# Performance work log

Hardware: AMD Instinct MI355X
Metric: run time of the kernel (lower is better)

Reference implementation:

```python
import jax, jax.numpy as jnp
import numpy as np

B, Q, K, DQ, DK, DV, H = 16, 64, 512, 512, 512, 512, 256
MASK_VAL = -1e6


def setup_inputs() -> dict:
    key = jax.random.key(0)
    k1, k2, k3, k4, k5, k6, k7 = jax.random.split(key, 7)
    return {
        "queries": jax.random.normal(k1, (B, Q, DQ), dtype=jnp.float32),
        "keys": jax.random.normal(k2, (B, K, DK), dtype=jnp.float32),
        "values": jax.random.normal(k3, (B, K, DV), dtype=jnp.float32),
        "valid_lens": jax.random.randint(k4, (B,), 1, K + 1, dtype=jnp.int32),
        "Wq": jax.random.normal(k5, (DQ, H), dtype=jnp.float32) * (1.0 / np.sqrt(DQ)),
        "Wk": jax.random.normal(k6, (DK, H), dtype=jnp.float32) * (1.0 / np.sqrt(DK)),
        "Wv": jax.random.normal(k7, (H,), dtype=jnp.float32) * (1.0 / np.sqrt(H)),
    }


def reference(queries, keys, values, valid_lens, Wq, Wk, Wv):
    # Project queries and keys into the shared additive-attention space.
    q = jnp.einsum("bqd,dh->bqh", queries, Wq)   # [B,Q,H]
    k = jnp.einsum("bkd,dh->bkh", keys, Wk)      # [B,K,H]
    # Bahdanau additive scoring: tanh(q + k) projected to a scalar per (q,k).
    feats = jnp.tanh(q[:, :, None, :] + k[:, None, :, :])  # [B,Q,K,H]
    scores = jnp.einsum("bqkh,h->bqk", feats, Wv)           # [B,Q,K]
    # Masked softmax over the key axis (positions >= valid_len masked out).
    mask = jnp.arange(K)[None, None, :] < valid_lens[:, None, None]  # [B,1,K]
    scores = jnp.where(mask, scores, MASK_VAL)
    attn = jax.nn.softmax(scores, axis=-1)                  # [B,Q,K]
    # Dropout is identity in eval mode; weighted sum of values.
    return jnp.einsum("bqk,bkv->bqv", attn, values)         # [B,Q,DV]
```

## Files before the change

kernel.cpp:

```cpp
#include <hip/hip_runtime.h>

#define LOG2E 1.4426950408889634f
#define TWO_LOG2E 2.8853900817779268f

typedef __attribute__((ext_vector_type(8))) short short8;
typedef __attribute__((ext_vector_type(4))) float f32x4;

__device__ __forceinline__ float e2x(float v) {
    return __builtin_amdgcn_exp2f(v * TWO_LOG2E);
}

__device__ __forceinline__ void split2(float x, float y, unsigned& hi, unsigned& lo) {
    unsigned ux = __float_as_uint(x), uy = __float_as_uint(y);
    float hx = __uint_as_float(ux & 0xffff0000u);
    float hy = __uint_as_float(uy & 0xffff0000u);
    unsigned lx = __float_as_uint(x - hx), ly = __float_as_uint(y - hy);
    hi = (ux >> 16) | (uy & 0xffff0000u);
    lo = (lx >> 16) | (ly & 0xffff0000u);
}

__global__ __launch_bounds__(256) void wprep_kernel(const float* __restrict__ Wq,
                                                    const float* __restrict__ Wk,
                                                    ushort* __restrict__ Wq2T,
                                                    ushort* __restrict__ Wk2T) {
    __shared__ float T[64][65];
    const float* W  = blockIdx.z ? Wk : Wq;
    ushort* W2T     = blockIdx.z ? Wk2T : Wq2T;
    const int t  = threadIdx.x;
    const int k0 = blockIdx.x * 64;
    const int n0 = blockIdx.y * 64;
#pragma unroll
    for (int p = 0; p < 4; ++p) {
        int u  = t + p * 256;
        int kk = u >> 4;
        int nf = (u & 15) * 4;
        float4 w = *reinterpret_cast<const float4*>(&W[(size_t)(k0 + kk) * 256 + n0 + nf]);
        T[nf + 0][kk] = w.x; T[nf + 1][kk] = w.y;
        T[nf + 2][kk] = w.z; T[nf + 3][kk] = w.w;
    }
    __syncthreads();
#pragma unroll
    for (int p = 0; p < 4; ++p) {
        int u  = t + p * 256;
        int n  = u >> 4;
        int kf = (u & 15) * 4;
        float a = T[n][kf], b = T[n][kf + 1], c = T[n][kf + 2], d = T[n][kf + 3];
        unsigned h01, l01, h23, l23;
        split2(a, b, h01, l01);
        split2(c, d, h23, l23);
        int kg = k0 + kf;
        ushort* row = W2T + (size_t)(n0 + n) * 1536 + (kg >> 5) * 96 + (kg & 31);
        uint2 hi; hi.x = h01; hi.y = h23;
        uint2 lo; lo.x = l01; lo.y = l23;
        *reinterpret_cast<uint2*>(row)      = hi;
        *reinterpret_cast<uint2*>(row + 32) = hi;
        *reinterpret_cast<uint2*>(row + 64) = lo;
    }
}

__global__ __launch_bounds__(256) void mfma_proj_kernel(const float* __restrict__ queries,
                                                        const float* __restrict__ keys,
                                                        const ushort* __restrict__ Wq2T,
                                                        const ushort* __restrict__ Wk2T,
                                                        float* __restrict__ Eq,
                                                        float* __restrict__ Ekp) {
    __shared__ float smemf[7680];
    ushort* Ah = reinterpret_cast<ushort*>(smemf);
    ushort* Ws = reinterpret_cast<ushort*>(smemf) + 3072;

    const int t    = threadIdx.x;
    const int mt   = blockIdx.x;
    const int Nb   = blockIdx.y * 128;
    const bool isQ = mt < 32;
    const int mloc = (isQ ? mt : mt - 32) * 32;
    const float4* Asrc4 = reinterpret_cast<const float4*>(isQ ? queries : keys)
                        + (size_t)mloc * 128;
    const ushort* W2T = isQ ? Wq2T : Wk2T;

    const int ln15 = t & 15;
    const int q    = (t >> 4) & 3;
    const int w    = t >> 6;
    const int wn   = w * 32;

    const char* gB[6];
#pragma unroll
    for (int i = 0; i < 6; ++i) {
        int o   = i * 4096 + t * 16;
        int row = o / 192;
        int rem = o - row * 192;
        gB[i] = reinterpret_cast<const char*>(W2T) + (size_t)(Nb + row) * 3072 + rem;
    }

    f32x4 acc[2][2];
#pragma unroll
    for (int fm = 0; fm < 2; ++fm)
#pragma unroll
        for (int fn = 0; fn < 2; ++fn) acc[fm][fn] = (f32x4)0.0f;

    for (int c = 0; c < 16; ++c) {
        __syncthreads();
        {
            int m  = t >> 3;
            int kf = (t & 7) * 4;
            float4 a = Asrc4[(size_t)m * 128 + c * 8 + (t & 7)];
            unsigned h01, l01, h23, l23;
            split2(a.x, a.y, h01, l01);
            split2(a.z, a.w, h23, l23);
            uint2 hi; hi.x = h01; hi.y = h23;
            uint2 lo; lo.x = l01; lo.y = l23;
            ushort* row = Ah + m * 96 + kf;
            *reinterpret_cast<uint2*>(row)      = hi;
            *reinterpret_cast<uint2*>(row + 32) = lo;
            *reinterpret_cast<uint2*>(row + 64) = hi;
        }
#pragma unroll
        for (int i = 0; i < 6; ++i) {
            __builtin_amdgcn_global_load_lds(
                reinterpret_cast<const unsigned int*>(gB[i]),
                reinterpret_cast<unsigned int*>(
                    reinterpret_cast<char*>(Ah) + 6144 + i * 4096 + (t >> 6) * 1024),
                16, 0, 0);
            gB[i] += 192;
        }
        __syncthreads();
#pragma unroll
        for (int s = 0; s < 3; ++s) {
            short8 af[2], bf[2];
#pragma unroll
            for (int fm = 0; fm < 2; ++fm)
                af[fm] = *reinterpret_cast<const short8*>(
                    Ah + (fm * 16 + ln15) * 96 + s * 32 + q * 8);
#pragma unroll
            for (int fn = 0; fn < 2; ++fn)
                bf[fn] = *reinterpret_cast<const short8*>(
                    Ws + (wn + fn * 16 + ln15) * 96 + s * 32 + q * 8);
#pragma unroll
            for (int fm = 0; fm < 2; ++fm)
#pragma unroll
                for (int fn = 0; fn < 2; ++fn)
                    acc[fm][fn] = __builtin_amdgcn_mfma_f32_16x16x32_bf16(
                        af[fm], bf[fn], acc[fm][fn], 0, 0, 0);
        }
    }

    if (isQ) {
#pragma unroll
        for (int fm = 0; fm < 2; ++fm)
#pragma unroll
            for (int fn = 0; fn < 2; ++fn)
#pragma unroll
                for (int r = 0; r < 4; ++r) {
                    int row = mloc + fm * 16 + q * 4 + r;
                    int col = Nb + wn + fn * 16 + ln15;
                    Eq[(size_t)row * 256 + col] = e2x(acc[fm][fn][r]);
                }
    } else {
        __syncthreads();
        float (*Cs)[33] = reinterpret_cast<float(*)[33]>(smemf);
#pragma unroll
        for (int fm = 0; fm < 2; ++fm)
#pragma unroll
            for (int fn = 0; fn < 2; ++fn)
#pragma unroll
                for (int r = 0; r < 4; ++r) {
                    int m_l = fm * 16 + q * 4 + r;
                    int n_l = wn + fn * 16 + ln15;
                    Cs[n_l][m_l] = acc[fm][fn][r];
                }
        __syncthreads();
        const int b      = mloc >> 9;
        const int k0h    = (mloc & 511) >> 1;
        const int h2base = Nb >> 1;
        float4* out4 = reinterpret_cast<float4*>(Ekp);
#pragma unroll
        for (int p = 0; p < 4; ++p) {
            int u   = t + p * 256;
            int h2r = u >> 4;
            int kp  = u & 15;
            int kk  = kp * 2;
            float4 o;
            o.x = e2x(Cs[2 * h2r    ][kk    ]);
            o.y = e2x(Cs[2 * h2r + 1][kk    ]);
            o.z = e2x(Cs[2 * h2r    ][kk + 1]);
            o.w = e2x(Cs[2 * h2r + 1][kk + 1]);
            out4[(size_t)b * 32768 + (size_t)(h2base + h2r) * 256 + k0h + kp] = o;
        }
    }
}

__global__ __launch_bounds__(256) void score_softmax_kernel(
        const float* __restrict__ Eq, const float* __restrict__ Ekp,
        const float* __restrict__ Wv, const int* __restrict__ valid_lens,
        float* __restrict__ attn) {
    __shared__ float redmA[4], redmB[4], redlA[4], redlB[4];

    const int t  = threadIdx.x;
    const int bq = blockIdx.x;
    const int b  = bq >> 5;
    const int q0 = (bq & 31) * 2;

    const float* eqA = Eq + (size_t)(b * 64 + q0) * 256;
    const float* eqB = eqA + 256;
    const float4* ek4 = reinterpret_cast<const float4*>(Ekp) + (size_t)b * 32768 + t;

    float accA0 = 0.f, accA1 = 0.f, accB0 = 0.f, accB1 = 0.f;
#pragma unroll 4
    for (int h2 = 0; h2 < 128; ++h2) {
        const float4 ek = ek4[h2 * 256];
        const float w0 = Wv[2 * h2];
        const float w1 = Wv[2 * h2 + 1];
        {
            const float e0 = eqA[2 * h2], e1 = eqA[2 * h2 + 1];
            float a00 = fmaf(e0, ek.x, 1.0f);
            float a10 = fmaf(e1, ek.y, 1.0f);
            float a01 = fmaf(e0, ek.z, 1.0f);
            float a11 = fmaf(e1, ek.w, 1.0f);
            float d0 = a00 * a10, d1 = a01 * a11;
            float n0 = fmaf(w1, a00, w0 * a10);
            float n1 = fmaf(w1, a01, w0 * a11);
            accA0 = fmaf(n0, __builtin_amdgcn_rcpf(d0), accA0);
            accA1 = fmaf(n1, __builtin_amdgcn_rcpf(d1), accA1);
        }
        {
            const float e0 = eqB[2 * h2], e1 = eqB[2 * h2 + 1];
            float a00 = fmaf(e0, ek.x, 1.0f);
            float a10 = fmaf(e1, ek.y, 1.0f);
            float a01 = fmaf(e0, ek.z, 1.0f);
            float a11 = fmaf(e1, ek.w, 1.0f);
            float d0 = a00 * a10, d1 = a01 * a11;
            float n0 = fmaf(w1, a00, w0 * a10);
            float n1 = fmaf(w1, a01, w0 * a11);
            accB0 = fmaf(n0, __builtin_amdgcn_rcpf(d0), accB0);
            accB1 = fmaf(n1, __builtin_amdgcn_rcpf(d1), accB1);
        }
    }
    float sA0 = -2.0f * accA0, sA1 = -2.0f * accA1;
    float sB0 = -2.0f * accB0, sB1 = -2.0f * accB1;
    const int vl = valid_lens[b];
    const int k0 = 2 * t;
    if (k0     >= vl) { sA0 = -1e6f; sB0 = -1e6f; }
    if (k0 + 1 >= vl) { sA1 = -1e6f; sB1 = -1e6f; }

    const int w = t >> 6;
    float mA = fmaxf(sA0, sA1);
    float mB = fmaxf(sB0, sB1);
#pragma unroll
    for (int off = 32; off > 0; off >>= 1) {
        mA = fmaxf(mA, __shfl_xor(mA, off));
        mB = fmaxf(mB, __shfl_xor(mB, off));
    }
    if ((t & 63) == 0) { redmA[w] = mA; redmB[w] = mB; }
    __syncthreads();
    mA = fmaxf(fmaxf(redmA[0], redmA[1]), fmaxf(redmA[2], redmA[3]));
    mB = fmaxf(fmaxf(redmB[0], redmB[1]), fmaxf(redmB[2], redmB[3]));

    float pA0 = __builtin_amdgcn_exp2f((sA0 - mA) * LOG2E);
    float pA1 = __builtin_amdgcn_exp2f((sA1 - mA) * LOG2E);
    float pB0 = __builtin_amdgcn_exp2f((sB0 - mB) * LOG2E);
    float pB1 = __builtin_amdgcn_exp2f((sB1 - mB) * LOG2E);
    float lA = pA0 + pA1, lB = pB0 + pB1;
#pragma unroll
    for (int off = 32; off > 0; off >>= 1) {
        lA += __shfl_xor(lA, off);
        lB += __shfl_xor(lB, off);
    }
    if ((t & 63) == 0) { redlA[w] = lA; redlB[w] = lB; }
    __syncthreads();
    lA = (redlA[0] + redlA[1]) + (redlA[2] + redlA[3]);
    lB = (redlB[0] + redlB[1]) + (redlB[2] + redlB[3]);
    const float invA = 1.0f / lA;
    const float invB = 1.0f / lB;

    float2* attn2 = reinterpret_cast<float2*>(attn);
    float2 oA; oA.x = pA0 * invA; oA.y = pA1 * invA;
    float2 oB; oB.x = pB0 * invB; oB.y = pB1 * invB;
    attn2[(size_t)(b * 64 + q0) * 256 + t]       = oA;
    attn2[(size_t)(b * 64 + q0 + 1) * 256 + t]   = oB;
}

__global__ __launch_bounds__(256) void pv_kernel(const float* __restrict__ attn,
                                                 const float* __restrict__ values,
                                                 float* __restrict__ out) {
    __shared__ __align__(16) float Ps[8][516];
    __shared__ __align__(16) float Vs[64][128];

    const int t  = threadIdx.x;
    const int b  = blockIdx.z;
    const int q0 = blockIdx.y * 8;
    const int vt = blockIdx.x;

    const float4* attn4 = reinterpret_cast<const float4*>(attn) + (size_t)(b * 64 + q0) * 128;
#pragma unroll
    for (int p = 0; p < 4; ++p) {
        int u  = t + p * 256;
        int qr = u >> 7;
        int c4 = u & 127;
        *reinterpret_cast<float4*>(&Ps[qr][c4 * 4]) = attn4[(size_t)qr * 128 + c4];
    }

    const char* vbase = reinterpret_cast<const char*>(values)
                      + ((size_t)b * 512 * 512 + (size_t)vt * 128) * 4
                      + (size_t)(t >> 5) * 2048 + (size_t)(t & 31) * 16;
    char* ldsV = reinterpret_cast<char*>(&Vs[0][0]) + (t >> 6) * 1024;

    const int lane = t & 63;
    const int w    = t >> 6;
    const int v4   = lane & 31;
    const int ksub = lane >> 5;

    float4 acc0 = make_float4(0.f, 0.f, 0.f, 0.f);
    float4 acc1 = make_float4(0.f, 0.f, 0.f, 0.f);

    for (int c = 0; c < 8; ++c) {
#pragma unroll
        for (int i = 0; i < 8; ++i) {
            __builtin_amdgcn_global_load_lds(
                reinterpret_cast<const unsigned int*>(
                    vbase + (size_t)c * 131072 + (size_t)i * 8 * 2048),
                reinterpret_cast<unsigned int*>(ldsV + i * 4096),
                16, 0, 0);
        }
        __syncthreads();

        const float* pr0 = &Ps[2 * w][c * 64];
        const float* pr1 = &Ps[2 * w + 1][c * 64];
#pragma unroll
        for (int kk = 0; kk < 8; ++kk) {
            int kb = kk * 8 + ksub * 4;
            float4 V0 = *reinterpret_cast<const float4*>(&Vs[kb + 0][v4 * 4]);
            float4 V1 = *reinterpret_cast<const float4*>(&Vs[kb + 1][v4 * 4]);
            float4 V2 = *reinterpret_cast<const float4*>(&Vs[kb + 2][v4 * 4]);
            float4 V3 = *reinterpret_cast<const float4*>(&Vs[kb + 3][v4 * 4]);
            float4 p0 = *reinterpret_cast<const float4*>(&pr0[kb]);
            float4 p1 = *reinterpret_cast<const float4*>(&pr1[kb]);
            acc0.x = fmaf(p0.x, V0.x, acc0.x); acc0.y = fmaf(p0.x, V0.y, acc0.y);
            acc0.z = fmaf(p0.x, V0.z, acc0.z); acc0.w = fmaf(p0.x, V0.w, acc0.w);
            acc0.x = fmaf(p0.y, V1.x, acc0.x); acc0.y = fmaf(p0.y, V1.y, acc0.y);
            acc0.z = fmaf(p0.y, V1.z, acc0.z); acc0.w = fmaf(p0.y, V1.w, acc0.w);
            acc0.x = fmaf(p0.z, V2.x, acc0.x); acc0.y = fmaf(p0.z, V2.y, acc0.y);
            acc0.z = fmaf(p0.z, V2.z, acc0.z); acc0.w = fmaf(p0.z, V2.w, acc0.w);
            acc0.x = fmaf(p0.w, V3.x, acc0.x); acc0.y = fmaf(p0.w, V3.y, acc0.y);
            acc0.z = fmaf(p0.w, V3.z, acc0.z); acc0.w = fmaf(p0.w, V3.w, acc0.w);
            acc1.x = fmaf(p1.x, V0.x, acc1.x); acc1.y = fmaf(p1.x, V0.y, acc1.y);
            acc1.z = fmaf(p1.x, V0.z, acc1.z); acc1.w = fmaf(p1.x, V0.w, acc1.w);
            acc1.x = fmaf(p1.y, V1.x, acc1.x); acc1.y = fmaf(p1.y, V1.y, acc1.y);
            acc1.z = fmaf(p1.y, V1.z, acc1.z); acc1.w = fmaf(p1.y, V1.w, acc1.w);
            acc1.x = fmaf(p1.z, V2.x, acc1.x); acc1.y = fmaf(p1.z, V2.y, acc1.y);
            acc1.z = fmaf(p1.z, V2.z, acc1.z); acc1.w = fmaf(p1.z, V2.w, acc1.w);
            acc1.x = fmaf(p1.w, V3.x, acc1.x); acc1.y = fmaf(p1.w, V3.y, acc1.y);
            acc1.z = fmaf(p1.w, V3.z, acc1.z); acc1.w = fmaf(p1.w, V3.w, acc1.w);
        }
        __syncthreads();
    }

    acc0.x += __shfl_xor(acc0.x, 32); acc0.y += __shfl_xor(acc0.y, 32);
    acc0.z += __shfl_xor(acc0.z, 32); acc0.w += __shfl_xor(acc0.w, 32);
    acc1.x += __shfl_xor(acc1.x, 32); acc1.y += __shfl_xor(acc1.y, 32);
    acc1.z += __shfl_xor(acc1.z, 32); acc1.w += __shfl_xor(acc1.w, 32);
    if (ksub == 0) {
        float4* out4 = reinterpret_cast<float4*>(out);
        out4[(size_t)(b * 64 + q0 + 2 * w) * 128 + vt * 32 + v4]     = acc0;
        out4[(size_t)(b * 64 + q0 + 2 * w + 1) * 128 + vt * 32 + v4] = acc1;
    }
}

extern "C" void kernel_launch(void* const* d_in, const int* in_sizes, int n_in,
                              void* d_out, int out_size, void* d_ws, size_t ws_size,
                              hipStream_t stream) {
    (void)in_sizes; (void)n_in; (void)out_size; (void)ws_size;
    const float* queries    = (const float*)d_in[0];
    const float* keys       = (const float*)d_in[1];
    const float* values     = (const float*)d_in[2];
    const int*   valid_lens = (const int*)d_in[3];
    const float* Wq         = (const float*)d_in[4];
    const float* Wk         = (const float*)d_in[5];
    const float* Wv         = (const float*)d_in[6];
    float* out = (float*)d_out;

    float* ws    = (float*)d_ws;
    float* Eq    = ws;
    float* Ekp   = ws + 262144;
    float* attn  = ws + 262144 + 2097152;
    ushort* Wq2T = (ushort*)(ws + 2883584);
    ushort* Wk2T = Wq2T + 393216;

    hipLaunchKernelGGL(wprep_kernel, dim3(8, 4, 2), dim3(256), 0, stream,
                       Wq, Wk, Wq2T, Wk2T);
    hipLaunchKernelGGL(mfma_proj_kernel, dim3(288, 2), dim3(256), 0, stream,
                       queries, keys, Wq2T, Wk2T, Eq, Ekp);
    hipLaunchKernelGGL(score_softmax_kernel, dim3(512), dim3(256), 0, stream,
                       Eq, Ekp, Wv, valid_lens, attn);
    hipLaunchKernelGGL(pv_kernel, dim3(4, 8, 16), dim3(256), 0, stream, attn, values, out);
}
```

Before: 141.1 us.

## Prefetch A tiles in projection kernel and double-buffer V tiles in PV kernel

In the projection GEMM, the next A chunk is now loaded from global memory into registers during the current iteration, and the bf16 split/store to LDS is placed after the W loads are issued. In the PV kernel, the V staging buffer is split into two 32-row halves so the next chunk's global-to-LDS load is issued while the current chunk is computed. The aim is to hide global memory latency behind compute. The cost is extra registers, and the PV loop's synchronisation must now protect buffer reuse correctly; the visible part of the loop does not show a barrier before the next chunk's load.

```diff
diff --git a/kernel.cpp b/kernel.cpp
--- a/kernel.cpp
+++ b/kernel.cpp
@@ -81,6 +81,8 @@
     const int q    = (t >> 4) & 3;
     const int w    = t >> 6;
     const int wn   = w * 32;
+    const int am   = t >> 3;
+    const int ak   = t & 7;
 
     const char* gB[6];
 #pragma unroll
@@ -97,22 +99,10 @@
 #pragma unroll
         for (int fn = 0; fn < 2; ++fn) acc[fm][fn] = (f32x4)0.0f;
 
+    float4 ra = Asrc4[(size_t)am * 128 + ak];
+
     for (int c = 0; c < 16; ++c) {
         __syncthreads();
-        {
-            int m  = t >> 3;
-            int kf = (t & 7) * 4;
-            float4 a = Asrc4[(size_t)m * 128 + c * 8 + (t & 7)];
-            unsigned h01, l01, h23, l23;
-            split2(a.x, a.y, h01, l01);
-            split2(a.z, a.w, h23, l23);
-            uint2 hi; hi.x = h01; hi.y = h23;
-            uint2 lo; lo.x = l01; lo.y = l23;
-            ushort* row = Ah + m * 96 + kf;
-            *reinterpret_cast<uint2*>(row)      = hi;
-            *reinterpret_cast<uint2*>(row + 32) = lo;
-            *reinterpret_cast<uint2*>(row + 64) = hi;
-        }
 #pragma unroll
         for (int i = 0; i < 6; ++i) {
             __builtin_amdgcn_global_load_lds(
@@ -122,6 +112,18 @@
                 16, 0, 0);
             gB[i] += 192;
         }
+        {
+            unsigned h01, l01, h23, l23;
+            split2(ra.x, ra.y, h01, l01);
+            split2(ra.z, ra.w, h23, l23);
+            uint2 hi; hi.x = h01; hi.y = h23;
+            uint2 lo; lo.x = l01; lo.y = l23;
+            ushort* row = Ah + am * 96 + ak * 4;
+            *reinterpret_cast<uint2*>(row)      = hi;
+            *reinterpret_cast<uint2*>(row + 32) = lo;
+            *reinterpret_cast<uint2*>(row + 64) = hi;
+        }
+        if (c < 15) ra = Asrc4[(size_t)am * 128 + (c + 1) * 8 + ak];
         __syncthreads();
 #pragma unroll
         for (int s = 0; s < 3; ++s) {
@@ -282,7 +284,7 @@
                                                  const float* __restrict__ values,
                                                  float* __restrict__ out) {
     __shared__ __align__(16) float Ps[8][516];
-    __shared__ __align__(16) float Vs[64][128];
+    __shared__ __align__(16) float Vs[2][32][128];
 
     const int t  = threadIdx.x;
     const int b  = blockIdx.z;
@@ -301,7 +303,7 @@
     const char* vbase = reinterpret_cast<const char*>(values)
                       + ((size_t)b * 512 * 512 + (size_t)vt * 128) * 4
                       + (size_t)(t >> 5) * 2048 + (size_t)(t & 31) * 16;
-    char* ldsV = reinterpret_cast<char*>(&Vs[0][0]) + (t >> 6) * 1024;
+    char* ldsV0 = reinterpret_cast<char*>(&Vs[0][0][0]) + (t >> 6) * 1024;
 
     const int lane = t & 63;
     const int w    = t >> 6;
@@ -311,26 +313,34 @@
     float4 acc0 = make_float4(0.f, 0.f, 0.f, 0.f);
     float4 acc1 = make_float4(0.f, 0.f, 0.f, 0.f);
 
-    for (int c = 0; c < 8; ++c) {
-#pragma unroll
-        for (int i = 0; i < 8; ++i) {
-            __builtin_amdgcn_global_load_lds(
-                reinterpret_cast<const unsigned int*>(
-                    vbase + (size_t)c * 131072 + (size_t)i * 8 * 2048),
-                reinterpret_cast<unsigned int*>(ldsV + i * 4096),
-                16, 0, 0);
-        }
-        __syncthreads();
-
-        const float* pr0 = &Ps[2 * w][c * 64];
-        const float* pr1 = &Ps[2 * w + 1][c * 64];
-#pragma unroll
-        for (int kk = 0; kk < 8; ++kk) {
+#pragma unroll
+    for (int i = 0; i < 4; ++i)
+        __builtin_amdgcn_global_load_lds(
+            reinterpret_cast<const unsigned int*>(vbase + (size_t)i * 8 * 2048),
+            reinterpret_cast<unsigned int*>(ldsV0 + i * 4096), 16, 0, 0);
+    __syncthreads();
+
+    for (int c = 0; c < 16; ++c) {
+        if (c < 15) {
+            char* dst = reinterpret_cast<char*>(&Vs[(c + 1) & 1][0][0]) + (t >> 6) * 1024;
+            const char* src = vbase + (size_t)(c + 1) * 65536;
+#pragma unroll
+            for (int i = 0; i < 4; ++i)
+                __builtin_amdgcn_global_load_lds(
+                    reinterpret_cast<const unsigned int*>(src + (size_t)i * 8 * 2048),
+                    reinterpret_cast<unsigned int*>(dst + i * 4096), 16, 0, 0);
+        }
+
+        const float (*V)[128] = Vs[c & 1];
+        const float* pr0 = &Ps[2 * w][c * 32];
+        const float* pr1 = &Ps[2 * w + 1][c * 32];
+#pragma unroll
+        for (int kk = 0; kk < 4; ++kk) {
             int kb = kk * 8 + ksub * 4;
-            float4 V0 = *reinterpret_cast<const float4*>(&Vs[kb + 0][v4 * 4]);
-            float4 V1 = *reinterpret_cast<const float4*>(&Vs[kb + 1][v4 * 4]);
-            float4 V2 = *reinterpret_cast<const float4*>(&Vs[kb + 2][v4 * 4]);
-            float4 V3 = *reinterpret_cast<const float4*>(&Vs[kb + 3][v4 * 4]);
+            float4 V0 = *reinterpret_cast<const float4*>(&V[kb + 0][v4 * 4]);
+            float4 V1 = *reinterpret_cast<const float4*>(&V[kb + 1][v4 * 4]);
+            float4 V2 = *reinterpret_cast<const float4*>(&V[kb + 2][v4 * 4]);
+            float4 V3 = *reinterpret_cast<const float4*>(&V[kb + 3][v4 * 4]);
             float4 p0 = *reinterpret_cast<const float4*>(&pr0[kb]);
             float4 p1 = *reinterpret_cast<const float4*>(&pr1[kb]);
             acc0.x = fmaf(p0.x, V0.x, acc0.x); acc0.y = fmaf(p0.x, V0.y, acc0.y);
```

Result: no change. 141.6 us (+0.4%).
